# Optimization experiments

Measured on AMD Instinct MI355X. Metric: run time of the kernel, lower is better.

The kernel has to match this reference:

```python
import jax, jax.numpy as jnp
import numpy as np

EPS = 1e-5

def bn_ncl(x, g, b):
    # BatchNorm1d over [n, C, L] (train mode, biased var), channel axis = 1
    m = x.mean(axis=(0, 2), keepdims=True)
    v = x.var(axis=(0, 2), keepdims=True)
    return (x - m) * jax.lax.rsqrt(v + EPS) * g[None, :, None] + b[None, :, None]

def bn_nc(x, g, b):
    # BatchNorm1d over [n, C] (train mode, biased var)
    m = x.mean(axis=0, keepdims=True)
    v = x.var(axis=0, keepdims=True)
    return (x - m) * jax.lax.rsqrt(v + EPS) * g + b

def mlp_head(x, w, b, g, bt):
    # Linear -> ReLU -> BatchNorm1d
    return bn_nc(jax.nn.relu(x @ w.T + b), g, bt)

def setup_inputs() -> dict:
    key = jax.random.key(0)
    ks = jax.random.split(key, 32)
    n, R, F, L = 2048, 116, 3, 4
    H = 128
    DN, DE = R * F, R * R  # 348, 13456
    s = 0.05  # xavier-like small scale
    f32 = jnp.float32
    return {
        "X": jax.random.normal(ks[0], (n, R, F), f32),
        "Z": jax.random.uniform(ks[1], (n, R, R), f32),
        "conv1_w": jax.random.normal(ks[2], (L, F, F), f32) * s,
        "conv1_b": jnp.zeros((L, F), f32),
        "conv2_w": jax.random.normal(ks[3], (L, R, R), f32) * s,
        "conv2_b": jnp.zeros((L, R), f32),
        "node_w": jax.random.normal(ks[4], (L, F, F), f32),
        "edge_w": jax.random.normal(ks[5], (L, R, R), f32) * s,
        "bn_n_g": jnp.ones((L, R), f32),
        "bn_n_b": jnp.zeros((L, R), f32),
        "bn_e_g": jnp.ones((L, R), f32),
        "bn_e_b": jnp.zeros((L, R), f32),
        "ln_w": jax.random.normal(ks[6], (L + 1, H, DN), f32) * s,
        "ln_b": jnp.zeros((L + 1, H), f32),
        "ln_bn_g": jnp.ones((L + 1, H), f32),
        "ln_bn_b": jnp.zeros((L + 1, H), f32),
        "le_w": jax.random.normal(ks[7], (L + 1, 3 * H, DE), f32) * (s * 0.2),
        "le_b": jnp.zeros((L + 1, 3 * H), f32),
        "le_bn_g": jnp.ones((L + 1, 3 * H), f32),
        "le_bn_b": jnp.zeros((L + 1, 3 * H), f32),
        "c1_w": jax.random.normal(ks[8], (1024, 4 * H * (L + 1)), f32) * s,
        "c1_b": jnp.zeros((1024,), f32),
        "c2_w": jax.random.normal(ks[9], (2, 1024), f32) * s,
        "c2_b": jnp.zeros((2,), f32),
    }

def reference(X, Z, conv1_w, conv1_b, conv2_w, conv2_b, node_w, edge_w,
              bn_n_g, bn_n_b, bn_e_g, bn_e_b,
              ln_w, ln_b, ln_bn_g, ln_bn_b,
              le_w, le_b, le_bn_g, le_bn_b,
              c1_w, c1_b, c2_w, c2_b):
    n = X.shape[0]
    L = conv1_w.shape[0]
    XXs = [mlp_head(X.reshape(n, -1), ln_w[0], ln_b[0], ln_bn_g[0], ln_bn_b[0])]
    ZZs = [mlp_head(Z.reshape(n, -1), le_w[0], le_b[0], le_bn_g[0], le_bn_b[0])]
    for i in range(L):
        # Attention: K = conv1(X^T) [n,3,116]; Q = K^T; V = conv2(Z^T) [n,116,116]
        K = jnp.einsum('oi,nli->nol', conv1_w[i], X) + conv1_b[i][None, :, None]
        att = jax.nn.softmax(jnp.einsum('ncl,ncm->nlm', K, K), axis=-1)  # Q @ K
        V = jnp.einsum('oi,nli->nol', conv2_w[i], Z) + conv2_b[i][None, :, None]
        A = jnp.einsum('nlk,nkm->nml', att, V)  # bmm(att, V).permute(0,2,1)
        # edge branch
        Z2 = jnp.einsum('nij,njk,kl->nil', A, Z, edge_w[i])
        Z = jax.nn.relu(bn_ncl(Z2, bn_e_g[i], bn_e_b[i])) + Z
        ZZs.append(mlp_head(Z.reshape(n, -1), le_w[i + 1], le_b[i + 1], le_bn_g[i + 1], le_bn_b[i + 1]))
        # node branch
        X1 = jnp.einsum('nij,njk,kl->nil', A, X, node_w[i])
        X = jax.nn.relu(bn_ncl(X1, bn_n_g[i], bn_n_b[i])) + X
        XXs.append(mlp_head(X.reshape(n, -1), ln_w[i + 1], ln_b[i + 1], ln_bn_g[i + 1], ln_bn_b[i + 1]))
    XZ = jnp.concatenate(XXs + ZZs, axis=1)  # [n, 128*4*(L+1)]
    h = jax.nn.relu(XZ @ c1_w.T + c1_b)  # dropout = identity (eval)
    return h @ c2_w.T + c2_b
```

## Files before the change

kernel.cpp:

```cpp
#include <hip/hip_runtime.h>
#include <hip/hip_bf16.h>

#define NS  2048
#define RR  116
#define LLY 4
#define HD  128
#define DN  348
#define DE  13456
#define KH  16384
#define SP  136
#define XZC 2560
#define C1O 1024
#define EPSF 1e-5f

typedef __attribute__((ext_vector_type(8))) short short8;
typedef __attribute__((ext_vector_type(4))) float floatx4;

static __device__ __forceinline__ ushort f2bf(float x) {
  union { __hip_bfloat16 b; ushort u; } cv;
  cv.b = __float2bfloat16(x);
  return cv.u;
}
static __device__ __forceinline__ float bf2f(ushort u) {
  union { ushort u; __hip_bfloat16 b; } cv;
  cv.u = u;
  return __bfloat162float(cv.b);
}
static __device__ __forceinline__ float fexp2(float x) {
#if __has_builtin(__builtin_amdgcn_exp2f)
  return __builtin_amdgcn_exp2f(x);
#else
  return exp2f(x);
#endif
}

#define GLDS16(gsrc, ldst) __builtin_amdgcn_global_load_lds( \
    (const __attribute__((address_space(1))) unsigned int*)(gsrc), \
    (__attribute__((address_space(3))) unsigned int*)(ldst), 16, 0, 0)

__global__ __launch_bounds__(256) void gemm64(
    const float* __restrict__ A, int lda,
    const float* __restrict__ B, int ldb,
    const float* __restrict__ bias,
    float* __restrict__ C, int ldc, int cof,
    int M, int N, int K)
{
  const int m0 = blockIdx.y * 64, n0 = blockIdx.x * 64;
  __shared__ float As[16][68];
  __shared__ float Bs[16][68];
  const int t = threadIdx.x;
  const int tx = t & 15, ty = t >> 4;
  float acc[4][4] = {};
  for (int kb = 0; kb < K; kb += 16) {
    {
      int mm = t >> 2, kk = (t & 3) << 2;
      int gm = m0 + mm, gk = kb + kk;
      float4 v = make_float4(0.f, 0.f, 0.f, 0.f);
      if (gm < M && gk < K) v = *(const float4*)(A + (size_t)gm * lda + gk);
      As[kk + 0][mm] = v.x; As[kk + 1][mm] = v.y; As[kk + 2][mm] = v.z; As[kk + 3][mm] = v.w;
      int gn = n0 + mm;
      float4 u = make_float4(0.f, 0.f, 0.f, 0.f);
      if (gn < N && gk < K) u = *(const float4*)(B + (size_t)gn * ldb + gk);
      Bs[kk + 0][mm] = u.x; Bs[kk + 1][mm] = u.y; Bs[kk + 2][mm] = u.z; Bs[kk + 3][mm] = u.w;
    }
    __syncthreads();
#pragma unroll
    for (int kk = 0; kk < 16; kk++) {
      float4 av = *(const float4*)&As[kk][ty << 2];
      float4 bv = *(const float4*)&Bs[kk][tx << 2];
      acc[0][0] += av.x * bv.x; acc[0][1] += av.x * bv.y; acc[0][2] += av.x * bv.z; acc[0][3] += av.x * bv.w;
      acc[1][0] += av.y * bv.x; acc[1][1] += av.y * bv.y; acc[1][2] += av.y * bv.z; acc[1][3] += av.y * bv.w;
      acc[2][0] += av.z * bv.x; acc[2][1] += av.z * bv.y; acc[2][2] += av.z * bv.z; acc[2][3] += av.z * bv.w;
      acc[3][0] += av.w * bv.x; acc[3][1] += av.w * bv.y; acc[3][2] += av.w * bv.z; acc[3][3] += av.w * bv.w;
    }
    __syncthreads();
  }
#pragma unroll
  for (int i = 0; i < 4; i++) {
    int m = m0 + (ty << 2) + i;
#pragma unroll
    for (int j = 0; j < 4; j++) {
      int n = n0 + (tx << 2) + j;
      if (m < M && n < N)
        C[(size_t)m * ldc + cof + n] = fmaxf(acc[i][j] + bias[n], 0.f);
    }
  }
}

__global__ __launch_bounds__(256) void gemm_mfma_tn(
    const ushort* __restrict__ A, int lka,
    const ushort* __restrict__ B, int lkb,
    float* __restrict__ C, int ldc, int cof,
    int ktiles)
{
  __shared__ __align__(16) ushort As[128 * 32];
  __shared__ __align__(16) ushort Bs[128 * 32];
  const int t = threadIdx.x;
  const int m0 = blockIdx.y * 128, n0 = blockIdx.x * 128;
  const int kt0 = (int)((long long)ktiles * blockIdx.z / gridDim.z);
  const int kt1 = (int)((long long)ktiles * (blockIdx.z + 1) / gridDim.z);
  const int w = t >> 6, lane = t & 63;
  const int wm = (w >> 1) << 6, wn = (w & 1) << 6;
  const int fr = lane & 15, quad = lane >> 4;
  const int row0 = t >> 2, row1 = (t + 256) >> 2;
  const int ko = (t & 3) * 8;
  floatx4 acc[4][4] = {};
  for (int kt = kt0; kt < kt1; ++kt) {
    const int kb = kt * 32;
    GLDS16(A + (size_t)(m0 + row0) * lka + kb + ko, &As[(size_t)t * 8]);
    GLDS16(A + (size_t)(m0 + row1) * lka + kb + ko, &As[(size_t)(t + 256) * 8]);
    GLDS16(B + (size_t)(n0 + row0) * lkb + kb + ko, &Bs[(size_t)t * 8]);
    GLDS16(B + (size_t)(n0 + row1) * lkb + kb + ko, &Bs[(size_t)(t + 256) * 8]);
    __syncthreads();
    short8 af[4], bf[4];
#pragma unroll
    for (int i = 0; i < 4; i++)
      af[i] = *(const short8*)&As[(wm + i * 16 + fr) * 32 + quad * 8];
#pragma unroll
    for (int j = 0; j < 4; j++)
      bf[j] = *(const short8*)&Bs[(wn + j * 16 + fr) * 32 + quad * 8];
#pragma unroll
    for (int i = 0; i < 4; i++)
#pragma unroll
      for (int j = 0; j < 4; j++)
        acc[i][j] = __builtin_amdgcn_mfma_f32_16x16x32_bf16(af[i], bf[j], acc[i][j], 0, 0, 0);
    __syncthreads();
  }
#pragma unroll
  for (int i = 0; i < 4; i++) {
#pragma unroll
    for (int j = 0; j < 4; j++) {
      int n = n0 + wn + j * 16 + fr;
#pragma unroll
      for (int r = 0; r < 4; r++) {
        int m = m0 + wm + i * 16 + quad * 4 + r;
        atomicAdd(&C[(size_t)m * ldc + cof + n], acc[i][j][r]);
      }
    }
  }
}

__global__ __launch_bounds__(256) void fusedG12(
    const ushort* __restrict__ ZHi, const ushort* __restrict__ ZLo,
    const ushort* __restrict__ WHi, const ushort* __restrict__ WLo,
    const float* __restrict__ b2, const float* __restrict__ Kf,
    ushort* __restrict__ AHi, ushort* __restrict__ ALo,
    const float* __restrict__ Xg, const float* __restrict__ nw,
    float* __restrict__ X1)
{
  __shared__ __align__(16) ushort pool[2 * 128 * SP];
  ushort* VtHi = pool;
  ushort* VtLo = pool + 128 * SP;
  ushort* tAhi = pool;
  ushort* tAlo = pool + 4096;
  ushort* tBhi = pool + 8192;
  ushort* tBlo = pool + 12288;
  __shared__ float Ks0[128], Ks1[128], Ks2[128], Mrow[128], Minv[128];
  __shared__ float Xs[DN];
  const int s = blockIdx.x;
  const int t = threadIdx.x;
  if (t < 128) {
    const float* kf = Kf + (size_t)s * 384;
    const float lam = 1.2011224087864498f;
    Ks0[t] = kf[t] * lam; Ks1[t] = kf[128 + t] * lam; Ks2[t] = kf[256 + t] * lam;
  }
  for (int ii = t; ii < DN; ii += 256) Xs[ii] = Xg[(size_t)s * DN + ii];
  __syncthreads();
  if (t < 128) {
    if (t < RR) {
      float k0 = Ks0[t], k1 = Ks1[t], k2 = Ks2[t];
      float mx = -3.0e38f;
      for (int k = 0; k < RR; k++)
        mx = fmaxf(mx, k0 * Ks0[k] + k1 * Ks1[k] + k2 * Ks2[k]);
      float sm = 0.f;
      for (int k = 0; k < RR; k++)
        sm += fexp2(k0 * Ks0[k] + k1 * Ks1[k] + k2 * Ks2[k] - mx);
      Mrow[t] = mx; Minv[t] = 1.f / sm;
    } else { Mrow[t] = 0.f; Minv[t] = 0.f; }
  }
  const int w = t >> 6, lane = t & 63;
  const int wm = (w >> 1) << 6, wn = (w & 1) << 6;
  const int fr = lane & 15, quad = lane >> 4;
  const int r0 = t >> 2, c8 = (t & 3) * 8;
  floatx4 acc[4][4] = {};
  for (int kt = 0; kt < 4; kt++) {
    const int kb = kt * 32;
    const size_t go = (size_t)s * KH + (size_t)r0 * 128 + kb + c8;
    GLDS16(ZHi + go, &tAhi[t * 8]);
    GLDS16(ZHi + go + 64 * 128, &tAhi[2048 + t * 8]);
    GLDS16(ZLo + go, &tAlo[t * 8]);
    GLDS16(ZLo + go + 64 * 128, &tAlo[2048 + t * 8]);
    const size_t wo = (size_t)r0 * 128 + kb + c8;
    GLDS16(WHi + wo, &tBhi[t * 8]);
    GLDS16(WHi + wo + 64 * 128, &tBhi[2048 + t * 8]);
    GLDS16(WLo + wo, &tBlo[t * 8]);
    GLDS16(WLo + wo + 64 * 128, &tBlo[2048 + t * 8]);
    __syncthreads();
    short8 ah[4], al[4], bh[4], bl[4];
#pragma unroll
    for (int i = 0; i < 4; i++) {
      ah[i] = *(const short8*)&tAhi[(wm + i * 16 + fr) * 32 + quad * 8];
      al[i] = *(const short8*)&tAlo[(wm + i * 16 + fr) * 32 + quad * 8];
    }
#pragma unroll
    for (int j = 0; j < 4; j++) {
      bh[j] = *(const short8*)&tBhi[(wn + j * 16 + fr) * 32 + quad * 8];
      bl[j] = *(const short8*)&tBlo[(wn + j * 16 + fr) * 32 + quad * 8];
    }
#pragma unroll
    for (int i = 0; i < 4; i++)
#pragma unroll
      for (int j = 0; j < 4; j++) {
        acc[i][j] = __builtin_amdgcn_mfma_f32_16x16x32_bf16(ah[i], bh[j], acc[i][j], 0, 0, 0);
        acc[i][j] = __builtin_amdgcn_mfma_f32_16x16x32_bf16(al[i], bh[j], acc[i][j], 0, 0, 0);
        acc[i][j] = __builtin_amdgcn_mfma_f32_16x16x32_bf16(ah[i], bl[j], acc[i][j], 0, 0, 0);
      }
    __syncthreads();
  }
#pragma unroll
  for (int i = 0; i < 4; i++) {
#pragma unroll
    for (int j = 0; j < 4; j++) {
      int n = wn + j * 16 + fr;
      float bb = (n < RR) ? b2[n] : 0.f;
#pragma unroll
      for (int r = 0; r < 4; r++) {
        int m = wm + i * 16 + quad * 4 + r;
        float v = acc[i][j][r] + bb;
        ushort h = f2bf(v);
        VtHi[m * SP + n] = h;
        VtLo[m * SP + n] = f2bf(v - bf2f(h));
      }
    }
  }
  __syncthreads();
  float Lk0[4], Lk1[4], Lk2[4], Lnm[4];
#pragma unroll
  for (int j = 0; j < 4; j++) {
    int l = wn + j * 16 + fr;
    Lk0[j] = Ks0[l]; Lk1[j] = Ks1[l]; Lk2[j] = Ks2[l]; Lnm[j] = -Mrow[l];
  }
  floatx4 ac2[4][4] = {};
  for (int kt = 0; kt < 4; kt++) {
    const int kb = kt * 32;
    float K0e[8], K1e[8], K2e[8];
#pragma unroll
    for (int e = 0; e < 8; e++) {
      int k = kb + quad * 8 + e;
      K0e[e] = Ks0[k]; K1e[e] = Ks1[k]; K2e[e] = Ks2[k];
    }
    short8 ah[4], al[4];
#pragma unroll
    for (int i = 0; i < 4; i++) {
      ah[i] = *(const short8*)&VtHi[(wm + i * 16 + fr) * SP + kb + quad * 8];
      al[i] = *(const short8*)&VtLo[(wm + i * 16 + fr) * SP + kb + quad * 8];
    }
#pragma unroll
    for (int j = 0; j < 4; j++) {
      short8 bh, bl;
#pragma unroll
      for (int e = 0; e < 8; e++) {
        float d = fmaf(Lk0[j], K0e[e], Lnm[j]);
        d = fmaf(Lk1[j], K1e[e], d);
        d = fmaf(Lk2[j], K2e[e], d);
        float a = fexp2(d);
        ushort h = f2bf(a);
        ((ushort*)&bh)[e] = h;
        ((ushort*)&bl)[e] = f2bf(a - bf2f(h));
      }
#pragma unroll
      for (int i = 0; i < 4; i++) {
        ac2[i][j] = __builtin_amdgcn_mfma_f32_16x16x32_bf16(ah[i], bh, ac2[i][j], 0, 0, 0);
        ac2[i][j] = __builtin_amdgcn_mfma_f32_16x16x32_bf16(al[i], bh, ac2[i][j], 0, 0, 0);
        ac2[i][j] = __builtin_amdgcn_mfma_f32_16x16x32_bf16(ah[i], bl, ac2[i][j], 0, 0, 0);
      }
    }
  }
  __syncthreads();
  float* Af = (float*)pool;
  ushort* CH = AHi + (size_t)s * KH;
  ushort* CL = ALo + (size_t)s * KH;
#pragma unroll
  for (int i = 0; i < 4; i++) {
#pragma unroll
    for (int j = 0; j < 4; j++) {
      int n = wn + j * 16 + fr;
      float iv = Minv[n];
#pragma unroll
      for (int r = 0; r < 4; r++) {
        int m = wm + i * 16 + quad * 4 + r;
        float v = ac2[i][j][r] * iv;
        ushort h = f2bf(v);
        CH[m * 128 + n] = h;
        CL[m * 128 + n] = f2bf(v - bf2f(h));
        Af[m * 133 + n] = v;
      }
    }
  }
  __syncthreads();
  if (t < RR) {
    float t0 = 0.f, t1 = 0.f, t2 = 0.f;
    const float* ar = Af + t * 133;
    for (int l = 0; l < RR; l++) {
      float p = ar[l];
      t0 += p * Xs[l * 3 + 0];
      t1 += p * Xs[l * 3 + 1];
      t2 += p * Xs[l * 3 + 2];
    }
    float n0 = nw[0], n1 = nw[1], n2 = nw[2];
    float n3 = nw[3], n4 = nw[4], n5 = nw[5];
    float n6 = nw[6], n7 = nw[7], n8 = nw[8];
    float* Op = X1 + (size_t)s * DN + t * 3;
    Op[0] = t0 * n0 + t1 * n3 + t2 * n6;
    Op[1] = t0 * n1 + t1 * n4 + t2 * n7;
    Op[2] = t0 * n2 + t1 * n5 + t2 * n8;
  }
}

__global__ __launch_bounds__(256) void fusedG34(
    const ushort* __restrict__ ZHi, const ushort* __restrict__ ZLo,
    const ushort* __restrict__ EHi, const ushort* __restrict__ ELo,
    ushort* __restrict__ AHi, ushort* __restrict__ ALo)
{
  __shared__ __align__(16) ushort pool[2 * 128 * SP];
  ushort* WtHi = pool;
  ushort* WtLo = pool + 128 * SP;
  ushort* tAhi = pool;
  ushort* tAlo = pool + 4096;
  ushort* tBhi = pool + 8192;
  ushort* tBlo = pool + 12288;
  const int s = blockIdx.x;
  const int t = threadIdx.x;
  const int w = t >> 6, lane = t & 63;
  const int wm = (w >> 1) << 6, wn = (w & 1) << 6;
  const int fr = lane & 15, quad = lane >> 4;
  const int r0 = t >> 2, c8 = (t & 3) * 8;
  floatx4 acc[4][4] = {};
  for (int kt = 0; kt < 4; kt++) {
    const int kb = kt * 32;
    const size_t go = (size_t)s * KH + (size_t)r0 * 128 + kb + c8;
    GLDS16(ZHi + go, &tAhi[t * 8]);
    GLDS16(ZHi + go + 64 * 128, &tAhi[2048 + t * 8]);
    GLDS16(ZLo + go, &tAlo[t * 8]);
    GLDS16(ZLo + go + 64 * 128, &tAlo[2048 + t * 8]);
    const size_t eo = (size_t)r0 * 128 + kb + c8;
    GLDS16(EHi + eo, &tBhi[t * 8]);
    GLDS16(EHi + eo + 64 * 128, &tBhi[2048 + t * 8]);
    GLDS16(ELo + eo, &tBlo[t * 8]);
    GLDS16(ELo + eo + 64 * 128, &tBlo[2048 + t * 8]);
    __syncthreads();
    short8 ah[4], al[4], bh[4], bl[4];
#pragma unroll
    for (int i = 0; i < 4; i++) {
      ah[i] = *(const short8*)&tAhi[(wm + i * 16 + fr) * 32 + quad * 8];
      al[i] = *(const short8*)&tAlo[(wm + i * 16 + fr) * 32 + quad * 8];
    }
#pragma unroll
    for (int j = 0; j < 4; j++) {
      bh[j] = *(const short8*)&tBhi[(wn + j * 16 + fr) * 32 + quad * 8];
      bl[j] = *(const short8*)&tBlo[(wn + j * 16 + fr) * 32 + quad * 8];
    }
#pragma unroll
    for (int i = 0; i < 4; i++)
#pragma unroll
      for (int j = 0; j < 4; j++) {
        acc[i][j] = __builtin_amdgcn_mfma_f32_16x16x32_bf16(ah[i], bh[j], acc[i][j], 0, 0, 0);
        acc[i][j] = __builtin_amdgcn_mfma_f32_16x16x32_bf16(al[i], bh[j], acc[i][j], 0, 0, 0);
        acc[i][j] = __builtin_amdgcn_mfma_f32_16x16x32_bf16(ah[i], bl[j], acc[i][j], 0, 0, 0);
      }
    __syncthreads();
  }
#pragma unroll
  for (int i = 0; i < 4; i++) {
#pragma unroll
    for (int j = 0; j < 4; j++) {
      int n = wn + j * 16 + fr;
      int mb = wm + i * 16 + quad * 4;
      ushort4 ph, pl;
#pragma unroll
      for (int r = 0; r < 4; r++) {
        float v = acc[i][j][r];
        ushort h = f2bf(v);
        ((ushort*)&ph)[r] = h;
        ((ushort*)&pl)[r] = f2bf(v - bf2f(h));
      }
      *(ushort4*)&WtHi[n * SP + mb] = ph;
      *(ushort4*)&WtLo[n * SP + mb] = pl;
    }
  }
  __syncthreads();
  const ushort* GAh = AHi + (size_t)s * KH;
  const ushort* GAl = ALo + (size_t)s * KH;
  floatx4 ac2[4][4] = {};
  for (int kt = 0; kt < 4; kt++) {
    const int kb = kt * 32;
    short8 ah[4], al[4], bh[4], bl[4];
#pragma unroll
    for (int i = 0; i < 4; i++) {
      const size_t ro = (size_t)(wm + i * 16 + fr) * 128 + kb + quad * 8;
      ah[i] = *(const short8*)(GAh + ro);
      al[i] = *(const short8*)(GAl + ro);
    }
#pragma unroll
    for (int j = 0; j < 4; j++) {
      bh[j] = *(const short8*)&WtHi[(wn + j * 16 + fr) * SP + kb + quad * 8];
      bl[j] = *(const short8*)&WtLo[(wn + j * 16 + fr) * SP + kb + quad * 8];
    }
#pragma unroll
    for (int i = 0; i < 4; i++)
#pragma unroll
      for (int j = 0; j < 4; j++) {
        ac2[i][j] = __builtin_amdgcn_mfma_f32_16x16x32_bf16(ah[i], bh[j], ac2[i][j], 0, 0, 0);
        ac2[i][j] = __builtin_amdgcn_mfma_f32_16x16x32_bf16(al[i], bh[j], ac2[i][j], 0, 0, 0);
        ac2[i][j] = __builtin_amdgcn_mfma_f32_16x16x32_bf16(ah[i], bl[j], ac2[i][j], 0, 0, 0);
      }
  }
  __syncthreads();
  ushort* CH = AHi + (size_t)s * KH;
  ushort* CL = ALo + (size_t)s * KH;
#pragma unroll
  for (int i = 0; i < 4; i++) {
#pragma unroll
    for (int j = 0; j < 4; j++) {
      int n = wn + j * 16 + fr;
#pragma unroll
      for (int r = 0; r < 4; r++) {
        int m = wm + i * 16 + quad * 4 + r;
        float v = ac2[i][j][r];
        ushort h = f2bf(v);
        CH[m * 128 + n] = h;
        CL[m * 128 + n] = f2bf(v - bf2f(h));
      }
    }
  }
}

__global__ void kprep(const float* __restrict__ Xb, const float* __restrict__ kw,
                      const float* __restrict__ kb, float* __restrict__ Kf)
{
  int idx = blockIdx.x * 256 + threadIdx.x;
  if (idx >= NS * 384) return;
  int s = idx / 384, r = idx - s * 384;
  int c = r >> 7, l = r & 127;
  float v = 0.f;
  if (l < RR) {
    const float* xp = Xb + (size_t)s * DN + l * 3;
    v = kw[c * 3 + 0] * xp[0] + kw[c * 3 + 1] * xp[1] + kw[c * 3 + 2] * xp[2] + kb[c];
  }
  Kf[idx] = v;
}

__global__ __launch_bounds__(256) void cvtZ0(
    const float* __restrict__ Z, ushort* __restrict__ ZHi, ushort* __restrict__ ZLo)
{
  const int s = blockIdx.x;
  const float* Zp = Z + (size_t)s * DE;
  ushort* h = ZHi + (size_t)s * KH;
  ushort* lo = ZLo + (size_t)s * KH;
  for (int idx = threadIdx.x; idx < KH; idx += 256) {
    int l = idx >> 7, i = idx & 127;
    if ((l < RR) && (i < RR)) {
      float v = Zp[l * RR + i];
      ushort hh = f2bf(v);
      h[idx] = hh; lo[idx] = f2bf(v - bf2f(hh));
    } else { h[idx] = 0; lo[idx] = 0; }
  }
}

__global__ void wprep2(const float* __restrict__ w2, const float* __restrict__ ew,
                       ushort* __restrict__ w2Hi, ushort* __restrict__ w2Lo,
                       ushort* __restrict__ eHi, ushort* __restrict__ eLo)
{
  int idx = blockIdx.x * 256 + threadIdx.x;
  int ly = idx >> 14, k = idx & (KH - 1);
  int r = k >> 7, c = k & 127;
  bool v = (r < RR) && (c < RR);
  float a = v ? w2[ly * DE + r * RR + c] : 0.f;
  float b = v ? ew[ly * DE + c * RR + r] : 0.f;
  ushort ha = f2bf(a), hb = f2bf(b);
  w2Hi[idx] = ha; w2Lo[idx] = f2bf(a - bf2f(ha));
  eHi[idx] = hb; eLo[idx] = f2bf(b - bf2f(hb));
}

__global__ void lewprep(const float* __restrict__ src, ushort* __restrict__ dst)
{
  int idx = blockIdx.x * 256 + threadIdx.x;
  int h = idx >> 14, k = idx & (KH - 1);
  int l = k >> 7, i = k & 127;
  bool v = (l < RR) && (i < RR);
  dst[idx] = v ? f2bf(src[(size_t)h * DE + l * RR + i]) : (ushort)0;
}

__global__ void cvt_pad(const float* __restrict__ src, ushort* __restrict__ dst,
                        long long total)
{
  long long idx = (long long)blockIdx.x * 256 + threadIdx.x;
  if (idx < total) dst[idx] = f2bf(src[idx]);
}

__global__ __launch_bounds__(256) void colstats(
    const float* __restrict__ Y, int ldy, int cof, int ncols, int chunk,
    float* __restrict__ sum, float* __restrict__ sq)
{
  const int cl = threadIdx.x & 63;
  const int c = blockIdx.x * 64 + cl;
  const int r4 = threadIdx.x >> 6;
  const int s0 = blockIdx.y * chunk;
  float a = 0.f, q = 0.f;
  if (c < ncols) {
    for (int r = s0 + r4; r < s0 + chunk; r += 4) {
      float v = Y[(size_t)r * ldy + cof + c];
      a += v; q += v * v;
    }
  }
  __shared__ float la[4][64], lq[4][64];
  la[r4][cl] = a; lq[r4][cl] = q;
  __syncthreads();
  if (threadIdx.x < 64) {
    int cc = blockIdx.x * 64 + threadIdx.x;
    if (cc < ncols) {
      float aa = la[0][threadIdx.x] + la[1][threadIdx.x] + la[2][threadIdx.x] + la[3][threadIdx.x];
      float qq = lq[0][threadIdx.x] + lq[1][threadIdx.x] + lq[2][threadIdx.x] + lq[3][threadIdx.x];
      atomicAdd(&sum[cc], aa);
      atomicAdd(&sq[cc], qq);
    }
  }
}

__global__ __launch_bounds__(256) void headpost(
    float* __restrict__ Y, int ldy, int cof, int ncols, int chunk,
    const float* __restrict__ bias,
    float* __restrict__ sum, float* __restrict__ sq)
{
  const int cl = threadIdx.x & 63;
  const int c = blockIdx.x * 64 + cl;
  const int r4 = threadIdx.x >> 6;
  const int s0 = blockIdx.y * chunk;
  float a = 0.f, q = 0.f;
  if (c < ncols) {
    float bb = bias[c];
    for (int r = s0 + r4; r < s0 + chunk; r += 4) {
      size_t o = (size_t)r * ldy + cof + c;
      float v = fmaxf(Y[o] + bb, 0.f);
      Y[o] = v;
      a += v; q += v * v;
    }
  }
  __shared__ float la[4][64], lq[4][64];
  la[r4][cl] = a; lq[r4][cl] = q;
  __syncthreads();
  if (threadIdx.x < 64) {
    int cc = blockIdx.x * 64 + threadIdx.x;
    if (cc < ncols) {
      float aa = la[0][threadIdx.x] + la[1][threadIdx.x] + la[2][threadIdx.x] + la[3][threadIdx.x];
      float qq = lq[0][threadIdx.x] + lq[1][threadIdx.x] + lq[2][threadIdx.x] + lq[3][threadIdx.x];
      atomicAdd(&sum[cc], aa);
      atomicAdd(&sq[cc], qq);
    }
  }
}

template<int NC>
__global__ void colnormb(const float* __restrict__ Y, ushort* __restrict__ Yb,
                         int ldy, int cof, float rinv,
                         const float* __restrict__ sum, const float* __restrict__ sq,
                         const float* __restrict__ g, const float* __restrict__ b,
                         unsigned total)
{
  unsigned idx = blockIdx.x * 256u + threadIdx.x;
  if (idx >= total) return;
  unsigned r = idx / NC, c = idx - r * NC;
  float m = sum[c] * rinv;
  float v = sq[c] * rinv - m * m;
  float iv = rsqrtf(v + EPSF);
  size_t o = (size_t)r * ldy + cof + c;
  Yb[o] = f2bf((Y[o] - m) * iv * g[c] + b[c]);
}

__global__ __launch_bounds__(256) void ncl_statsb_pair(
    const ushort* __restrict__ ZsHi, const ushort* __restrict__ ZsLo,
    float* __restrict__ sum, float* __restrict__ sq)
{
  const int c = blockIdx.x;
  const int s0 = blockIdx.y * 128;
  float a = 0.f, q = 0.f;
  for (int f = threadIdx.x; f < 2048; f += 256) {
    size_t off = (size_t)(s0 + (f >> 4)) * KH + c * 128 + (f & 15) * 8;
    const ushort* ph = ZsHi + off;
    const ushort* pl = ZsLo + off;
#pragma unroll
    for (int e = 0; e < 8; e++) {
      float v = bf2f(ph[e]) + bf2f(pl[e]);
      a += v; q += v * v;
    }
  }
  for (int o = 32; o; o >>= 1) { a += __shfl_down(a, o); q += __shfl_down(q, o); }
  __shared__ float pa[4], pq[4];
  const int wv = threadIdx.x >> 6;
  if ((threadIdx.x & 63) == 0) { pa[wv] = a; pq[wv] = q; }
  __syncthreads();
  if (threadIdx.x == 0) {
    atomicAdd(&sum[c], pa[0] + pa[1] + pa[2] + pa[3]);
    atomicAdd(&sq[c], pq[0] + pq[1] + pq[2] + pq[3]);
  }
}

__global__ void ncl_updatez_pair(
    ushort* __restrict__ ZHi, ushort* __restrict__ ZLo,
    const ushort* __restrict__ Z2Hi, const ushort* __restrict__ Z2Lo,
    const float* __restrict__ g, const float* __restrict__ b,
    const float* __restrict__ sum, const float* __restrict__ sq)
{
  unsigned idx = blockIdx.x * 256u + threadIdx.x;
  if (idx >= (unsigned)NS * DE) return;
  unsigned s = idx / DE, rem = idx - s * DE;
  unsigned i = rem / RR, l = rem - i * RR;
  size_t off = (size_t)s * KH + i * 128 + l;
  const float invcnt = 1.f / (float)(NS * RR);
  float m = sum[i] * invcnt;
  float v = sq[i] * invcnt - m * m;
  float iv = rsqrtf(v + EPSF);
  float z2 = bf2f(Z2Hi[off]) + bf2f(Z2Lo[off]);
  float z = (z2 - m) * iv * g[i] + b[i];
  float nv = bf2f(ZHi[off]) + bf2f(ZLo[off]) + fmaxf(z, 0.f);
  ushort h = f2bf(nv);
  ZHi[off] = h;
  ZLo[off] = f2bf(nv - bf2f(h));
}

template<int LC>
__global__ __launch_bounds__(256) void ncl_stats(
    const float* __restrict__ Xv, float* __restrict__ sum, float* __restrict__ sq)
{
  const int c = blockIdx.x;
  const int s0 = blockIdx.y * 128;
  const int tot = 128 * LC;
  float a = 0.f, q = 0.f;
  for (int f = threadIdx.x; f < tot; f += 256) {
    int sl = f / LC, l = f - sl * LC;
    float v = Xv[((size_t)(s0 + sl) * RR + c) * LC + l];
    a += v; q += v * v;
  }
  for (int o = 32; o; o >>= 1) { a += __shfl_down(a, o); q += __shfl_down(q, o); }
  __shared__ float pa[4], pq[4];
  const int wv = threadIdx.x >> 6;
  if ((threadIdx.x & 63) == 0) { pa[wv] = a; pq[wv] = q; }
  __syncthreads();
  if (threadIdx.x == 0) {
    atomicAdd(&sum[c], pa[0] + pa[1] + pa[2] + pa[3]);
    atomicAdd(&sq[c], pq[0] + pq[1] + pq[2] + pq[3]);
  }
}

template<int LC>
__global__ void ncl_update(float* __restrict__ dst, const float* __restrict__ src,
                           const float* __restrict__ g, const float* __restrict__ b,
                           const float* __restrict__ sum, const float* __restrict__ sq,
                           float invcnt, unsigned total)
{
  unsigned idx = blockIdx.x * 256u + threadIdx.x;
  if (idx >= total) return;
  int c = (int)((idx / LC) % RR);
  float m = sum[c] * invcnt;
  float v = sq[c] * invcnt - m * m;
  float iv = rsqrtf(v + EPSF);
  float z = (src[idx] - m) * iv * g[c] + b[c];
  dst[idx] += fmaxf(z, 0.f);
}

__global__ void hpost(float* __restrict__ Hh, const float* __restrict__ b, unsigned total)
{
  unsigned idx = blockIdx.x * 256u + threadIdx.x;
  if (idx >= total) return;
  Hh[idx] = fmaxf(Hh[idx] + b[idx & (C1O - 1)], 0.f);
}

__global__ __launch_bounds__(256) void c2k(const float* __restrict__ Hh,
                                           const float* __restrict__ w,
                                           const float* __restrict__ b,
                                           float* __restrict__ out)
{
  const int s = blockIdx.x;
  float a0 = 0.f, a1 = 0.f;
  for (int j = threadIdx.x; j < C1O; j += 256) {
    float h = Hh[(size_t)s * C1O + j];
    a0 += h * w[j];
    a1 += h * w[C1O + j];
  }
  for (int o = 32; o; o >>= 1) { a0 += __shfl_down(a0, o); a1 += __shfl_down(a1, o); }
  __shared__ float p0[4], p1[4];
  const int wv = threadIdx.x >> 6;
  if ((threadIdx.x & 63) == 0) { p0[wv] = a0; p1[wv] = a1; }
  __syncthreads();
  if (threadIdx.x == 0) {
    out[s * 2 + 0] = p0[0] + p0[1] + p0[2] + p0[3] + b[0];
    out[s * 2 + 1] = p1[0] + p1[1] + p1[2] + p1[3] + b[1];
  }
}

extern "C" void kernel_launch(void* const* d_in, const int* in_sizes, int n_in,
                              void* d_out, int out_size, void* d_ws, size_t ws_size,
                              hipStream_t stream)
{
  const float* X    = (const float*)d_in[0];
  const float* Z    = (const float*)d_in[1];
  const float* cv1w = (const float*)d_in[2];
  const float* cv1b = (const float*)d_in[3];
  const float* cv2w = (const float*)d_in[4];
  const float* cv2b = (const float*)d_in[5];
  const float* nw   = (const float*)d_in[6];
  const float* ew   = (const float*)d_in[7];
  const float* bng  = (const float*)d_in[8];
  const float* bnb  = (const float*)d_in[9];
  const float* beg  = (const float*)d_in[10];
  const float* beb  = (const float*)d_in[11];
  const float* lnw  = (const float*)d_in[12];
  const float* lnb  = (const float*)d_in[13];
  const float* lng  = (const float*)d_in[14];
  const float* lnbt = (const float*)d_in[15];
  const float* lew  = (const float*)d_in[16];
  const float* leb  = (const float*)d_in[17];
  const float* leg  = (const float*)d_in[18];
  const float* lebt = (const float*)d_in[19];
  const float* fc1w = (const float*)d_in[20];
  const float* fc1b = (const float*)d_in[21];
  const float* fc2w = (const float*)d_in[22];
  const float* fc2b = (const float*)d_in[23];
  float* out = (float*)d_out;

  char* base = (char*)d_ws;
  ushort* ZHi  = (ushort*)base;                     base += (size_t)NS * KH * 2;
  ushort* ZLo  = (ushort*)base;                     base += (size_t)NS * KH * 2;
  ushort* ARHi = (ushort*)base;                     base += (size_t)NS * KH * 2;
  ushort* ARLo = (ushort*)base;                     base += (size_t)NS * KH * 2;
  ushort* XZb  = (ushort*)base;                     base += (size_t)NS * XZC * 2;
  ushort* c1wh = (ushort*)base;                     base += (size_t)C1O * XZC * 2;
  ushort* lewh = (ushort*)base;                     base += (size_t)384 * KH * 2;
  ushort* w2Hi = (ushort*)base;                     base += (size_t)4 * KH * 2;
  ushort* w2Lo = (ushort*)base;                     base += (size_t)4 * KH * 2;
  ushort* eHi  = (ushort*)base;                     base += (size_t)4 * KH * 2;
  ushort* eLo  = (ushort*)base;                     base += (size_t)4 * KH * 2;
  float* Xb = (float*)base;                         base += (size_t)NS * DN * 4;
  float* X1 = (float*)base;                         base += (size_t)NS * DN * 4;
  float* XZ = (float*)base;                         base += (size_t)NS * XZC * 4;
  float* HH = (float*)base;                         base += (size_t)NS * C1O * 4;
  float* Kf = (float*)base;                         base += (size_t)NS * 384 * 4;
  float* ST = (float*)base;

  hipMemcpyAsync(Xb, X, sizeof(float) * (size_t)NS * DN, hipMemcpyDeviceToDevice, stream);
  hipMemsetAsync(XZ, 0, sizeof(float) * (size_t)NS * XZC, stream);
  hipMemsetAsync(HH, 0, sizeof(float) * (size_t)NS * C1O, stream);
  cvt_pad<<<(unsigned)(((long long)C1O * XZC + 255) / 256), 256, 0, stream>>>(
      fc1w, c1wh, (long long)C1O * XZC);
  wprep2<<<(4 * KH) / 256, 256, 0, stream>>>(cv2w, ew, w2Hi, w2Lo, eHi, eLo);
  cvtZ0<<<NS, 256, 0, stream>>>(Z, ZHi, ZLo);

  const float rinv = 1.f / (float)NS;

  auto head384 = [&](int hd, int cof) {
    lewprep<<<(384 * KH) / 256, 256, 0, stream>>>(lew + (size_t)hd * 384 * DE, lewh);
    gemm_mfma_tn<<<dim3(3, 16, 6), 256, 0, stream>>>(
        ZHi, KH, lewh, KH, XZ, XZC, cof, KH / 32);
    hipMemsetAsync(ST, 0, sizeof(float) * 768, stream);
    headpost<<<dim3(6, 8), 256, 0, stream>>>(XZ, XZC, cof, 384, 256,
                                             leb + hd * 384, ST, ST + 384);
    colnormb<384><<<(NS * 384 + 255) / 256, 256, 0, stream>>>(
        XZ, XZb, XZC, cof, rinv, ST, ST + 384, leg + hd * 384, lebt + hd * 384, NS * 384);
  };
  auto head128 = [&](int hd, int cof) {
    gemm64<<<dim3(2, NS / 64, 1), 256, 0, stream>>>(
        Xb, DN, lnw + (size_t)hd * HD * DN, DN, lnb + hd * HD, XZ, XZC, cof, NS, HD, DN);
    hipMemsetAsync(ST, 0, sizeof(float) * 768, stream);
    colstats<<<dim3(2, 8), 256, 0, stream>>>(XZ, XZC, cof, HD, 256, ST, ST + 384);
    colnormb<HD><<<(NS * HD + 255) / 256, 256, 0, stream>>>(
        XZ, XZb, XZC, cof, rinv, ST, ST + 384, lng + hd * HD, lnbt + hd * HD, NS * HD);
  };

  head128(0, 0);
  head384(0, 640);

  for (int i = 0; i < LLY; i++) {
    kprep<<<(NS * 384 + 255) / 256, 256, 0, stream>>>(Xb, cv1w + i * 9, cv1b + i * 3, Kf);
    fusedG12<<<NS, 256, 0, stream>>>(ZHi, ZLo, w2Hi + (size_t)i * KH, w2Lo + (size_t)i * KH,
                                     cv2b + i * RR, Kf, ARHi, ARLo,
                                     Xb, nw + i * 9, X1);
    fusedG34<<<NS, 256, 0, stream>>>(ZHi, ZLo, eHi + (size_t)i * KH, eLo + (size_t)i * KH,
                                     ARHi, ARLo);
    hipMemsetAsync(ST + 768, 0, sizeof(float) * 512, stream);
    ncl_statsb_pair<<<dim3(RR, 16), 256, 0, stream>>>(ARHi, ARLo, ST + 768, ST + 768 + 128);
    ncl_stats<3><<<dim3(RR, 16), 256, 0, stream>>>(X1, ST + 768 + 256, ST + 768 + 384);
    ncl_updatez_pair<<<((unsigned)NS * DE + 255) / 256, 256, 0, stream>>>(
        ZHi, ZLo, ARHi, ARLo, beg + i * RR, beb + i * RR, ST + 768, ST + 768 + 128);
    ncl_update<3><<<((unsigned)NS * DN + 255) / 256, 256, 0, stream>>>(
        Xb, X1, bng + i * RR, bnb + i * RR, ST + 768 + 256, ST + 768 + 384,
        1.f / (float)(NS * 3), (unsigned)NS * DN);
    head384(i + 1, 640 + (i + 1) * 384);
    head128(i + 1, (i + 1) * HD);
  }

  gemm_mfma_tn<<<dim3(C1O / 128, NS / 128, 2), 256, 0, stream>>>(
      XZb, XZC, c1wh, XZC, HH, C1O, 0, XZC / 32);
  hpost<<<((unsigned)NS * C1O + 255) / 256, 256, 0, stream>>>(HH, fc1b, (unsigned)NS * C1O);
  c2k<<<NS, 256, 0, stream>>>(HH, fc2w, fc2b, out);
}
```

Before: 2.605 ms.

## Fuse BatchNorm stats into attention kernels, double-buffer MFMA tiles, add split-K

Per-channel sum and sum-of-squares for both BatchNorm branches are now accumulated with atomics in the epilogues of fusedG12 and fusedG34. This removes the separate ncl_statsb_pair and ncl_stats passes that reread the large intermediate tensors. gemm_mfma_tn, fusedG12 and fusedG34 now double-buffer their LDS tiles so the next tile's loads overlap the current MFMAs. The softmax prologue also overlaps with the first tile load. gemm64 gains split-K with atomic accumulation, with bias and ReLU moved into headpost, and split-K factors are raised for the other GEMMs. The tradeoff is more atomic traffic and more LDS per block.

```diff
diff --git a/kernel.cpp b/kernel.cpp
--- a/kernel.cpp
+++ b/kernel.cpp
@@ -41,17 +41,20 @@
 __global__ __launch_bounds__(256) void gemm64(
     const float* __restrict__ A, int lda,
     const float* __restrict__ B, int ldb,
-    const float* __restrict__ bias,
     float* __restrict__ C, int ldc, int cof,
     int M, int N, int K)
 {
   const int m0 = blockIdx.y * 64, n0 = blockIdx.x * 64;
+  const int ktiles = (K + 15) >> 4;
+  const int kt0 = (int)((long long)ktiles * blockIdx.z / gridDim.z);
+  const int kt1 = (int)((long long)ktiles * (blockIdx.z + 1) / gridDim.z);
   __shared__ float As[16][68];
   __shared__ float Bs[16][68];
   const int t = threadIdx.x;
   const int tx = t & 15, ty = t >> 4;
   float acc[4][4] = {};
-  for (int kb = 0; kb < K; kb += 16) {
+  for (int kt = kt0; kt < kt1; kt++) {
+    const int kb = kt * 16;
     {
       int mm = t >> 2, kk = (t & 3) << 2;
       int gm = m0 + mm, gk = kb + kk;
@@ -82,7 +85,7 @@
     for (int j = 0; j < 4; j++) {
       int n = n0 + (tx << 2) + j;
       if (m < M && n < N)
-        C[(size_t)m * ldc + cof + n] = fmaxf(acc[i][j] + bias[n], 0.f);
+        atomicAdd(&C[(size_t)m * ldc + cof + n], acc[i][j]);
     }
   }
 }
@@ -93,8 +96,8 @@
     float* __restrict__ C, int ldc, int cof,
     int ktiles)
 {
-  __shared__ __align__(16) ushort As[128 * 32];
-  __shared__ __align__(16) ushort Bs[128 * 32];
+  __shared__ __align__(16) ushort As[2][128 * 32];
+  __shared__ __align__(16) ushort Bs[2][128 * 32];
   const int t = threadIdx.x;
   const int m0 = blockIdx.y * 128, n0 = blockIdx.x * 128;
   const int kt0 = (int)((long long)ktiles * blockIdx.z / gridDim.z);
@@ -104,21 +107,26 @@
   const int fr = lane & 15, quad = lane >> 4;
   const int row0 = t >> 2, row1 = (t + 256) >> 2;
   const int ko = (t & 3) * 8;
+  auto stage = [&](int kt, int b) {
+    const int kb = kt * 32;
+    GLDS16(A + (size_t)(m0 + row0) * lka + kb + ko, &As[b][(size_t)t * 8]);
+    GLDS16(A + (size_t)(m0 + row1) * lka + kb + ko, &As[b][2048 + (size_t)t * 8]);
+    GLDS16(B + (size_t)(n0 + row0) * lkb + kb + ko, &Bs[b][(size_t)t * 8]);
+    GLDS16(B + (size_t)(n0 + row1) * lkb + kb + ko, &Bs[b][2048 + (size_t)t * 8]);
+  };
   floatx4 acc[4][4] = {};
+  stage(kt0, 0);
+  __syncthreads();
   for (int kt = kt0; kt < kt1; ++kt) {
-    const int kb = kt * 32;
-    GLDS16(A + (size_t)(m0 + row0) * lka + kb + ko, &As[(size_t)t * 8]);
-    GLDS16(A + (size_t)(m0 + row1) * lka + kb + ko, &As[(size_t)(t + 256) * 8]);
-    GLDS16(B + (size_t)(n0 + row0) * lkb + kb + ko, &Bs[(size_t)t * 8]);
-    GLDS16(B + (size_t)(n0 + row1) * lkb + kb + ko, &Bs[(size_t)(t + 256) * 8]);
-    __syncthreads();
+    const int cur = (kt - kt0) & 1;
+    if (kt + 1 < kt1) stage(kt + 1, cur ^ 1);
     short8 af[4], bf[4];
 #pragma unroll
     for (int i = 0; i < 4; i++)
-      af[i] = *(const short8*)&As[(wm + i * 16 + fr) * 32 + quad * 8];
+      af[i] = *(const short8*)&As[cur][(wm + i * 16 + fr) * 32 + quad * 8];
 #pragma unroll
     for (int j = 0; j < 4; j++)
-      bf[j] = *(const short8*)&Bs[(wn + j * 16 + fr) * 32 + quad * 8];
+      bf[j] = *(const short8*)&Bs[cur][(wn + j * 16 + fr) * 32 + quad * 8];
 #pragma unroll
     for (int i = 0; i < 4; i++)
 #pragma unroll
@@ -146,66 +154,73 @@
     const float* __restrict__ b2, const float* __restrict__ Kf,
     ushort* __restrict__ AHi, ushort* __restrict__ ALo,
     const float* __restrict__ Xg, const float* __restrict__ nw,
-    float* __restrict__ X1)
+    float* __restrict__ X1, float* __restrict__ xsum, float* __restrict__ xsq)
 {
   __shared__ __align__(16) ushort pool[2 * 128 * SP];
   ushort* VtHi = pool;
   ushort* VtLo = pool + 128 * SP;
-  ushort* tAhi = pool;
-  ushort* tAlo = pool + 4096;
-  ushort* tBhi = pool + 8192;
-  ushort* tBlo = pool + 12288;
   __shared__ float Ks0[128], Ks1[128], Ks2[128], Mrow[128], Minv[128];
   __shared__ float Xs[DN];
   const int s = blockIdx.x;
   const int t = threadIdx.x;
-  if (t < 128) {
-    const float* kf = Kf + (size_t)s * 384;
-    const float lam = 1.2011224087864498f;
-    Ks0[t] = kf[t] * lam; Ks1[t] = kf[128 + t] * lam; Ks2[t] = kf[256 + t] * lam;
-  }
-  for (int ii = t; ii < DN; ii += 256) Xs[ii] = Xg[(size_t)s * DN + ii];
-  __syncthreads();
-  if (t < 128) {
-    if (t < RR) {
-      float k0 = Ks0[t], k1 = Ks1[t], k2 = Ks2[t];
-      float mx = -3.0e38f;
-      for (int k = 0; k < RR; k++)
-        mx = fmaxf(mx, k0 * Ks0[k] + k1 * Ks1[k] + k2 * Ks2[k]);
-      float sm = 0.f;
-      for (int k = 0; k < RR; k++)
-        sm += fexp2(k0 * Ks0[k] + k1 * Ks1[k] + k2 * Ks2[k] - mx);
-      Mrow[t] = mx; Minv[t] = 1.f / sm;
-    } else { Mrow[t] = 0.f; Minv[t] = 0.f; }
-  }
   const int w = t >> 6, lane = t & 63;
   const int wm = (w >> 1) << 6, wn = (w & 1) << 6;
   const int fr = lane & 15, quad = lane >> 4;
   const int r0 = t >> 2, c8 = (t & 3) * 8;
+
+  auto stage = [&](int kt, int b) {
+    ushort* bb = pool + b * 16384;
+    const int kb = kt * 32;
+    const size_t go = (size_t)s * KH + (size_t)r0 * 128 + kb + c8;
+    GLDS16(ZHi + go,            bb + t * 8);
+    GLDS16(ZHi + go + 64 * 128, bb + 2048 + t * 8);
+    GLDS16(ZLo + go,            bb + 4096 + t * 8);
+    GLDS16(ZLo + go + 64 * 128, bb + 6144 + t * 8);
+    const size_t wo = (size_t)r0 * 128 + kb + c8;
+    GLDS16(WHi + wo,            bb + 8192 + t * 8);
+    GLDS16(WHi + wo + 64 * 128, bb + 10240 + t * 8);
+    GLDS16(WLo + wo,            bb + 12288 + t * 8);
+    GLDS16(WLo + wo + 64 * 128, bb + 14336 + t * 8);
+  };
+
+  stage(0, 0);
+  const float lam  = 1.2011224087864498f;
+  const float lam2 = 1.4426950408889634f;
+  if (t < 128) {
+    const float* kf = Kf + (size_t)s * 384;
+    Ks0[t] = kf[t] * lam; Ks1[t] = kf[128 + t] * lam; Ks2[t] = kf[256 + t] * lam;
+  }
+  for (int ii = t; ii < DN; ii += 256) Xs[ii] = Xg[(size_t)s * DN + ii];
+  if (t < 128) {
+    if (t < RR) {
+      const float* kf = Kf + (size_t)s * 384;
+      float k0 = kf[t] * lam2, k1 = kf[128 + t] * lam2, k2 = kf[256 + t] * lam2;
+      float mx = -3.0e38f;
+      for (int k = 0; k < RR; k++)
+        mx = fmaxf(mx, k0 * kf[k] + k1 * kf[128 + k] + k2 * kf[256 + k]);
+      float sm = 0.f;
+      for (int k = 0; k < RR; k++)
+        sm += fexp2(k0 * kf[k] + k1 * kf[128 + k] + k2 * kf[256 + k] - mx);
+      Mrow[t] = mx; Minv[t] = 1.f / sm;
+    } else { Mrow[t] = 0.f; Minv[t] = 0.f; }
+  }
+  __syncthreads();
+
   floatx4 acc[4][4] = {};
   for (int kt = 0; kt < 4; kt++) {
-    const int kb = kt * 32;
-    const size_t go = (size_t)s * KH + (size_t)r0 * 128 + kb + c8;
-    GLDS16(ZHi + go, &tAhi[t * 8]);
-    GLDS16(ZHi + go + 64 * 128, &tAhi[2048 + t * 8]);
-    GLDS16(ZLo + go, &tAlo[t * 8]);
-    GLDS16(ZLo + go + 64 * 128, &tAlo[2048 + t * 8]);
-    const size_t wo = (size_t)r0 * 128 + kb + c8;
-    GLDS16(WHi + wo, &tBhi[t * 8]);
-    GLDS16(WHi + wo + 64 * 128, &tBhi[2048 + t * 8]);
-    GLDS16(WLo + wo, &tBlo[t * 8]);
-    GLDS16(WLo + wo + 64 * 128, &tBlo[2048 + t * 8]);
-    __syncthreads();
+    const int cur = kt & 1;
+    if (kt < 3) stage(kt + 1, cur ^ 1);
+    const ushort* bb = pool + cur * 16384;
     short8 ah[4], al[4], bh[4], bl[4];
 #pragma unroll
     for (int i = 0; i < 4; i++) {
-      ah[i] = *(const short8*)&tAhi[(wm + i * 16 + fr) * 32 + quad * 8];
-      al[i] = *(const short8*)&tAlo[(wm + i * 16 + fr) * 32 + quad * 8];
-    }
-#pragma unroll
-    for (int j = 0; j < 4; j++) {
-      bh[j] = *(const short8*)&tBhi[(wn + j * 16 + fr) * 32 + quad * 8];
-      bl[j] = *(const short8*)&tBlo[(wn + j * 16 + fr) * 32 + quad * 8];
+      ah[i] = *(const short8*)&bb[(wm + i * 16 + fr) * 32 + quad * 8];
+      al[i] = *(const short8*)&bb[4096 + (wm + i * 16 + fr) * 32 + quad * 8];
+    }
+#pragma unroll
+    for (int j = 0; j < 4; j++) {
+      bh[j] = *(const short8*)&bb[8192 + (wn + j * 16 + fr) * 32 + quad * 8];
+      bl[j] = *(const short8*)&bb[12288 + (wn + j * 16 + fr) * 32 + quad * 8];
     }
 #pragma unroll
     for (int i = 0; i < 4; i++)
@@ -307,58 +322,64 @@
       t1 += p * Xs[l * 3 + 1];
       t2 += p * Xs[l * 3 + 2];
     }
-    float n0 = nw[0], n1 = nw[1], n2 = nw[2];
-    float n3 = nw[3], n4 = nw[4], n5 = nw[5];
-    float n6 = nw[6], n7 = nw[7], n8 = nw[8];
+    float o0 = t0 * nw[0] + t1 * nw[3] + t2 * nw[6];
+    float o1 = t0 * nw[1] + t1 * nw[4] + t2 * nw[7];
+    float o2 = t0 * nw[2] + t1 * nw[5] + t2 * nw[8];
     float* Op = X1 + (size_t)s * DN + t * 3;
-    Op[0] = t0 * n0 + t1 * n3 + t2 * n6;
-    Op[1] = t0 * n1 + t1 * n4 + t2 * n7;
-    Op[2] = t0 * n2 + t1 * n5 + t2 * n8;
+    Op[0] = o0; Op[1] = o1; Op[2] = o2;
+    atomicAdd(&xsum[t], o0 + o1 + o2);
+    atomicAdd(&xsq[t], o0 * o0 + o1 * o1 + o2 * o2);
   }
 }
 
 __global__ __launch_bounds__(256) void fusedG34(
     const ushort* __restrict__ ZHi, const ushort* __restrict__ ZLo,
     const ushort* __restrict__ EHi, const ushort* __restrict__ ELo,
-    ushort* __restrict__ AHi, ushort* __restrict__ ALo)
+    ushort* __restrict__ AHi, ushort* __restrict__ ALo,
+    float* __restrict__ zsum, float* __restrict__ zsq)
 {
   __shared__ __align__(16) ushort pool[2 * 128 * SP];
   ushort* WtHi = pool;
   ushort* WtLo = pool + 128 * SP;
-  ushort* tAhi = pool;
-  ushort* tAlo = pool + 4096;
-  ushort* tBhi = pool + 8192;
-  ushort* tBlo = pool + 12288;
   const int s = blockIdx.x;
   const int t = threadIdx.x;
   const int w = t >> 6, lane = t & 63;
   const int wm = (w >> 1) << 6, wn = (w & 1) << 6;
   const int fr = lane & 15, quad = lane >> 4;
   const int r0 = t >> 2, c8 = (t & 3) * 8;
-  floatx4 acc[4][4] = {};
-  for (int kt = 0; kt < 4; kt++) {
+
+  auto stage = [&](int kt, int b) {
+    ushort* bb = pool + b * 16384;
     const int kb = kt * 32;
     const size_t go = (size_t)s * KH + (size_t)r0 * 128 + kb + c8;
-    GLDS16(ZHi + go, &tAhi[t * 8]);
-    GLDS16(ZHi + go + 64 * 128, &tAhi[2048 + t * 8]);
-    GLDS16(ZLo + go, &tAlo[t * 8]);
-    GLDS16(ZLo + go + 64 * 128, &tAlo[2048 + t * 8]);
+    GLDS16(ZHi + go,            bb + t * 8);
+    GLDS16(ZHi + go + 64 * 128, bb + 2048 + t * 8);
+    GLDS16(ZLo + go,            bb + 4096 + t * 8);
+    GLDS16(ZLo + go + 64 * 128, bb + 6144 + t * 8);
     const size_t eo = (size_t)r0 * 128 + kb + c8;
-    GLDS16(EHi + eo, &tBhi[t * 8]);
-    GLDS16(EHi + eo + 64 * 128, &tBhi[2048 + t * 8]);
-    GLDS16(ELo + eo, &tBlo[t * 8]);
-    GLDS16(ELo + eo + 64 * 128, &tBlo[2048 + t * 8]);
-    __syncthreads();
+    GLDS16(EHi + eo,            bb + 8192 + t * 8);
+    GLDS16(EHi + eo + 64 * 128, bb + 10240 + t * 8);
+    GLDS16(ELo + eo,            bb + 12288 + t * 8);
+    GLDS16(ELo + eo + 64 * 128, bb + 14336 + t * 8);
+  };
+
+  floatx4 acc[4][4] = {};
+  stage(0, 0);
+  __syncthreads();
+  for (int kt = 0; kt < 4; kt++) {
+    const int cur = kt & 1;
+    if (kt < 3) stage(kt + 1, cur ^ 1);
+    const ushort* bb = pool + cur * 16384;
     short8 ah[4], al[4], bh[4], bl[4];
 #pragma unroll
     for (int i = 0; i < 4; i++) {
-      ah[i] = *(const short8*)&tAhi[(wm + i * 16 + fr) * 32 + quad * 8];
-      al[i] = *(const short8*)&tAlo[(wm + i * 16 + fr) * 32 + quad * 8];
-    }
-#pragma unroll
-    for (int j = 0; j < 4; j++) {
-      bh[j] = *(const short8*)&tBhi[(wn + j * 16 + fr) * 32 + quad * 8];
-      bl[j] = *(const short8*)&tBlo[(wn + j * 16 + fr) * 32 + quad * 8];
+      ah[i] = *(const short8*)&bb[(wm + i * 16 + fr) * 32 + quad * 8];
+      al[i] = *(const short8*)&bb[4096 + (wm + i * 16 + fr) * 32 + quad * 8];
+    }
+#pragma unroll
+    for (int j = 0; j < 4; j++) {
+      bh[j] = *(const short8*)&bb[8192 + (wn + j * 16 + fr) * 32 + quad * 8];
+      bl[j] = *(const short8*)&bb[12288 + (wn + j * 16 + fr) * 32 + quad * 8];
     }
 #pragma unroll
     for (int i = 0; i < 4; i++)
@@ -430,6 +451,24 @@
         ushort h = f2bf(v);
         CH[m * 128 + n] = h;
         CL[m * 128 + n] = f2bf(v - bf2f(h));
+      }
+    }
+  }
+#pragma unroll
+  for (int i = 0; i < 4; i++) {
+#pragma unroll
+    for (int r = 0; r < 4; r++) {
+      int m = wm + i * 16 + quad * 4 + r;
+      float a = 0.f, q = 0.f;
+#pragma unroll
+      for (int j = 0; j < 4; j++) { float v = ac2[i][j][r]; a += v; q += v * v; }
+      a += __shfl_xor(a, 1); q += __shfl_xor(q, 1);
+      a += __shfl_xor(a, 2); q += __shfl_xor(q, 2);
+      a += __shfl_xor(a, 4); q += __shfl_xor(q, 4);
+      a += __shfl_xor(a, 8); q += __shfl_xor(q, 8);
+      if ((lane & 15) == 0 && m < RR) {
+        atomicAdd(&zsum[m], a);
+        atomicAdd(&zsq[m], q);
       }
     }
   }
@@ -496,35 +535,6 @@
 {
   long long idx = (long long)blockIdx.x * 256 + threadIdx.x;
   if (idx < total) dst[idx] = f2bf(src[idx]);
-}
-
-__global__ __launch_bounds__(256) void colstats(
-    const float* __restrict__ Y, int ldy, int cof, int ncols, int chunk,
-    float* __restrict__ sum, float* __restrict__ sq)
-{
-  const int cl = threadIdx.x & 63;
-  const int c = blockIdx.x * 64 + cl;
-  const int r4 = threadIdx.x >> 6;
-  const int s0 = blockIdx.y * chunk;
-  float a = 0.f, q = 0.f;
-  if (c < ncols) {
-    for (int r = s0 + r4; r < s0 + chunk; r += 4) {
-      float v = Y[(size_t)r * ldy + cof + c];
-      a += v; q += v * v;
-    }
-  }
-  __shared__ float la[4][64], lq[4][64];
-  la[r4][cl] = a; lq[r4][cl] = q;
-  __syncthreads();
-  if (threadIdx.x < 64) {
-    int cc = blockIdx.x * 64 + threadIdx.x;
-    if (cc < ncols) {
-      float aa = la[0][threadIdx.x] + la[1][threadIdx.x] + la[2][threadIdx.x] + la[3][threadIdx.x];
-      float qq = lq[0][threadIdx.x] + lq[1][threadIdx.x] + lq[2][threadIdx.x] + lq[3][threadIdx.x];
-      atomicAdd(&sum[cc], aa);
-      atomicAdd(&sq[cc], qq);
-    }
-  }
 }
 
 __global__ __launch_bounds__(256) void headpost(
@@ -575,34 +585,6 @@
   float iv = rsqrtf(v + EPSF);
   size_t o = (size_t)r * ldy + cof + c;
   Yb[o] = f2bf((Y[o] - m) * iv * g[c] + b[c]);
-}
-
-__global__ __launch_bounds__(256) void ncl_statsb_pair(
-    const ushort* __restrict__ ZsHi, const ushort* __restrict__ ZsLo,
-    float* __restrict__ sum, float* __restrict__ sq)
-{
-  const int c = blockIdx.x;
-  const int s0 = blockIdx.y * 128;
-  float a = 0.f, q = 0.f;
-  for (int f = threadIdx.x; f < 2048; f += 256) {
-    size_t off = (size_t)(s0 + (f >> 4)) * KH + c * 128 + (f & 15) * 8;
-    const ushort* ph = ZsHi + off;
-    const ushort* pl = ZsLo + off;
-#pragma unroll
-    for (int e = 0; e < 8; e++) {
-      float v = bf2f(ph[e]) + bf2f(pl[e]);
-      a += v; q += v * v;
-    }
-  }
-  for (int o = 32; o; o >>= 1) { a += __shfl_down(a, o); q += __shfl_down(q, o); }
-  __shared__ float pa[4], pq[4];
-  const int wv = threadIdx.x >> 6;
-  if ((threadIdx.x & 63) == 0) { pa[wv] = a; pq[wv] = q; }
-  __syncthreads();
-  if (threadIdx.x == 0) {
-    atomicAdd(&sum[c], pa[0] + pa[1] + pa[2] + pa[3]);
-    atomicAdd(&sq[c], pq[0] + pq[1] + pq[2] + pq[3]);
-  }
 }
 
 __global__ void ncl_updatez_pair(
@@ -626,30 +608,6 @@
   ushort h = f2bf(nv);
   ZHi[off] = h;
   ZLo[off] = f2bf(nv - bf2f(h));
-}
-
-template<int LC>
-__global__ __launch_bounds__(256) void ncl_stats(
-    const float* __restrict__ Xv, float* __restrict__ sum, float* __restrict__ sq)
-{
-  const int c = blockIdx.x;
-  const int s0 = blockIdx.y * 128;
-  const int tot = 128 * LC;
-  float a = 0.f, q = 0.f;
-  for (int f = threadIdx.x; f < tot; f += 256) {
-    int sl = f / LC, l = f - sl * LC;
-    float v = Xv[((size_t)(s0 + sl) * RR + c) * LC + l];
-    a += v; q += v * v;
-  }
-  for (int o = 32; o; o >>= 1) { a += __shfl_down(a, o); q += __shfl_down(q, o); }
-  __shared__ float pa[4], pq[4];
-  const int wv = threadIdx.x >> 6;
-  if ((threadIdx.x & 63) == 0) { pa[wv] = a; pq[wv] = q; }
-  __syncthreads();
-  if (threadIdx.x == 0) {
-    atomicAdd(&sum[c], pa[0] + pa[1] + pa[2] + pa[3]);
-    atomicAdd(&sq[c], pq[0] + pq[1] + pq[2] + pq[3]);
-  }
 }
 
 template<int LC>
@@ -759,7 +717,7 @@
 
   auto head384 = [&](int hd, int cof) {
     lewprep<<<(384 * KH) / 256, 256, 0, stream>>>(lew + (size_t)hd * 384 * DE, lewh);
-    gemm_mfma_tn<<<dim3(3, 16, 6), 256, 0, stream>>>(
+    gemm_mfma_tn<<<dim3(3, 16, 12), 256, 0, stream>>>(
         ZHi, KH, lewh, KH, XZ, XZC, cof, KH / 32);
     hipMemsetAsync(ST, 0, sizeof(float) * 768, stream);
     headpost<<<dim3(6, 8), 256, 0, stream>>>(XZ, XZC, cof, 384, 256,
@@ -768,10 +726,11 @@
         XZ, XZb, XZC, cof, rinv, ST, ST + 384, leg + hd * 384, lebt + hd * 384, NS * 384);
   };
   auto head128 = [&](int hd, int cof) {
-    gemm64<<<dim3(2, NS / 64, 1), 256, 0, stream>>>(
-        Xb, DN, lnw + (size_t)hd * HD * DN, DN, lnb + hd * HD, XZ, XZC, cof, NS, HD, DN);
+    gemm64<<<dim3(2, NS / 64, 4), 256, 0, stream>>>(
+        Xb, DN, lnw + (size_t)hd * HD * DN, DN, XZ, XZC, cof, NS, HD, DN);
     hipMemsetAsync(ST, 0, sizeof(float) * 768, stream);
-    colstats<<<dim3(2, 8), 256, 0, stream>>>(XZ, XZC, cof, HD, 256, ST, ST + 384);
+    headpost<<<dim3(2, 8), 256, 0, stream>>>(XZ, XZC, cof, HD, 256,
+                                             lnb + hd * HD, ST, ST + 384);
     colnormb<HD><<<(NS * HD + 255) / 256, 256, 0, stream>>>(
         XZ, XZb, XZC, cof, rinv, ST, ST + 384, lng + hd * HD, lnbt + hd * HD, NS * HD);
   };
@@ -781,14 +740,13 @@
 
   for (int i = 0; i < LLY; i++) {
     kprep<<<(NS * 384 + 255) / 256, 256, 0, stream>>>(Xb, cv1w + i * 9, cv1b + i * 3, Kf);
+    hipMemsetAsync(ST + 768, 0, sizeof(float) * 512, stream);
     fusedG12<<<NS, 256, 0, stream>>>(ZHi, ZLo, w2Hi + (size_t)i * KH, w2Lo + (size_t)i * KH,
                                      cv2b + i * RR, Kf, ARHi, ARLo,
-                                     Xb, nw + i * 9, X1);
+                                     Xb, nw + i * 9, X1,
+                                     ST + 768 + 256, ST + 768 + 384);
     fusedG34<<<NS, 256, 0, stream>>>(ZHi, ZLo, eHi + (size_t)i * KH, eLo + (size_t)i * KH,
-                                     ARHi, ARLo);
-    hipMemsetAsync(ST + 768, 0, sizeof(float) * 512, stream);
-    ncl_statsb_pair<<<dim3(RR, 16), 256, 0, stream>>>(ARHi, ARLo, ST + 768, ST + 768 + 128);
-    ncl_stats<3><<<dim3(RR, 16), 256, 0, stream>>>(X1, ST + 768 + 256, ST + 768 + 384);
+                                     ARHi, ARLo, ST + 768, ST + 768 + 128);
     ncl_updatez_pair<<<((unsigned)NS * DE + 255) / 256, 256, 0, stream>>>(
         ZHi, ZLo, ARHi, ARLo, beg + i * RR, beb + i * RR, ST + 768, ST + 768 + 128);
     ncl_update<3><<<((unsigned)NS * DN + 255) / 256, 256, 0, stream>>>(
@@ -798,7 +756,7 @@
     head128(i + 1, (i + 1) * HD);
   }
 
-  gemm_mfma_tn<<<dim3(C1O / 128, NS / 128, 2), 256, 0, stream>>>(
+  gemm_mfma_tn<<<dim3(C1O / 128, NS / 128, 4), 256, 0, stream>>>(
       XZb, XZC, c1wh, XZC, HH, C1O, 0, XZC / 32);
   hpost<<<((unsigned)NS * C1O + 255) / 256, 256, 0, stream>>>(HH, fc1b, (unsigned)NS * C1O);
   c2k<<<NS, 256, 0, stream>>>(HH, fc2w, fc2b, out);
```

After: 3.807 ms. 1.46x slower.
